# Kernel optimization log

Hardware: AMD Instinct MI355X
Metric: run time of the kernel (lower is better)

The kernel has to match this reference:

```python
import jax, jax.numpy as jnp
import numpy as np

N_NODES = 50000
N_EDGES = 800000
NFEAT = 96
NHID = 96
NCLASS = 40


def setup_inputs() -> dict:
    key = jax.random.key(0)
    ks = jax.random.split(key, 8)
    x = jax.random.normal(ks[0], (N_NODES, NFEAT), dtype=jnp.float32)
    edge_index = jax.random.randint(ks[1], (2, N_EDGES), 0, N_NODES, dtype=jnp.int64)
    def glorot(k, shape):
        fan_in = shape[1]
        bound = 1.0 / np.sqrt(fan_in)
        return jax.random.uniform(k, shape, jnp.float32, -bound, bound)
    return {
        'x': x,
        'edge_index': edge_index,
        'W1_l': glorot(ks[2], (NHID, NFEAT)),
        'b1_l': jnp.zeros((NHID,), jnp.float32),
        'W1_r': glorot(ks[3], (NHID, NFEAT)),
        'W2_l': glorot(ks[4], (NCLASS, NHID)),
        'b2_l': jnp.zeros((NCLASS,), jnp.float32),
        'W2_r': glorot(ks[5], (NCLASS, NHID)),
    }


def _sage_conv(x, src, dst, W_l, b_l, W_r):
    # gather neighbor features per edge, scatter-mean onto dst nodes
    msg = x[src]                                   # [E, F]
    agg = jax.ops.segment_sum(msg, dst, num_segments=N_NODES)   # [N, F]
    cnt = jax.ops.segment_sum(jnp.ones((src.shape[0],), x.dtype), dst,
                              num_segments=N_NODES)             # [N]
    agg = agg / jnp.maximum(cnt, 1.0)[:, None]
    # lin_l(agg) + lin_r(x)
    return agg @ W_l.T + b_l + x @ W_r.T


def reference(x, edge_index, W1_l, b1_l, W1_r, W2_l, b2_l, W2_r):
    src, dst = edge_index[0], edge_index[1]
    h = _sage_conv(x, src, dst, W1_l, b1_l, W1_r)
    h = jax.nn.relu(h)  # dropout is identity in eval mode
    h = _sage_conv(h, src, dst, W2_l, b2_l, W2_r)
    return jax.nn.log_softmax(h, axis=1)
```

## Files before the change

kernel.cpp:

```cpp
#include <hip/hip_runtime.h>
#include <hip/hip_fp8.h>
#include <math.h>

#define NCLASS 40
#define BSH    6
#define BSIZE  64
#define MAXB   1024
#define BCAP   2048
#define EPB    4096
#define LCOL   2048

typedef __attribute__((ext_vector_type(8))) short short8;
typedef __attribute__((ext_vector_type(4))) float float4v;
typedef __attribute__((ext_vector_type(2))) float float2v;

__device__ __forceinline__ unsigned short f2bf(float f) {
    union { float f; unsigned u; } v; v.f = f;
    unsigned r = v.u + 0x7fffu + ((v.u >> 16) & 1u);
    return (unsigned short)(r >> 16);
}
__device__ __forceinline__ float bf2f(unsigned int s) {
    union { unsigned u; float f; } v; v.u = s << 16; return v.f;
}
__device__ __forceinline__ void acc_fp8x4(unsigned int v, float* a) {
#if __has_builtin(__builtin_amdgcn_cvt_pk_f32_fp8)
    float2v lo = __builtin_amdgcn_cvt_pk_f32_fp8((int)v, false);
    float2v hi = __builtin_amdgcn_cvt_pk_f32_fp8((int)v, true);
    a[0] += lo[0]; a[1] += lo[1]; a[2] += hi[0]; a[3] += hi[1];
#else
    #pragma unroll
    for (int k = 0; k < 4; ++k) {
        __hip_fp8_e4m3 q8; q8.__x = (__hip_fp8_storage_t)((v >> (8 * k)) & 0xffu);
        a[k] += (float)q8;
    }
#endif
}

__global__ __launch_bounds__(256) void convhist_kernel(const int* __restrict__ ei,
                                                       const float4* __restrict__ x4,
                                                       const float* __restrict__ W1l,
                                                       const float* __restrict__ W1r,
                                                       const float* __restrict__ W2l,
                                                       const float* __restrict__ W2r,
                                                       int* __restrict__ histT,
                                                       unsigned short* __restrict__ axb,
                                                       unsigned char* __restrict__ xq,
                                                       unsigned short* __restrict__ wb1,
                                                       unsigned short* __restrict__ wb2,
                                                       int N, int E, int nbucket,
                                                       int nbin, int xblocks) {
    __shared__ int hcnt[MAXB];
    int tid = threadIdx.x;
    int blk = blockIdx.x;
    if (blk < nbin) {
        for (int t = tid; t < nbucket; t += 256) hcnt[t] = 0;
        __syncthreads();
        int e0 = blk * EPB;
        for (int it = 0; it < EPB / 256; ++it) {
            int e = e0 + it * 256 + tid;
            if (e < E) atomicAdd(&hcnt[ei[E + e] >> BSH], 1);
        }
        __syncthreads();
        for (int t = tid; t < nbucket; t += 256)
            histT[t * nbin + blk] = hcnt[t];
        return;
    }
    if (blk < nbin + xblocks) {
        int idx = (blk - nbin) * 256 + tid;
        if (idx >= N * 24) return;
        int n = idx / 24, q = idx - n * 24;
        float4 v = x4[idx];
        ushort4 o;
        o.x = f2bf(v.x); o.y = f2bf(v.y); o.z = f2bf(v.z); o.w = f2bf(v.w);
        *(ushort4*)(axb + (size_t)n * 192 + 96 + q * 4) = o;
        __hip_fp8_e4m3 q0(v.x), q1(v.y), q2(v.z), q3(v.w);
        unsigned int pk = (unsigned)q0.__x | ((unsigned)q1.__x << 8)
                        | ((unsigned)q2.__x << 16) | ((unsigned)q3.__x << 24);
        *(unsigned int*)(xq + (size_t)n * 128 + q * 4) = pk;
        return;
    }
    int t = (blk - nbin - xblocks) * 256 + tid;
    const float* src;
    unsigned short* dst;
    if (t < 36 * 64) {
        int s = t >> 6, lane = t & 63;
        int kc = s / 6, jt = s - kc * 6;
        int j  = jt * 16 + (lane & 15);
        int k2 = kc * 32 + (lane >> 4) * 8;
        src = (k2 < 96) ? (W1l + j * 96 + k2) : (W1r + j * 96 + (k2 - 96));
        dst = wb1 + t * 8;
    } else if (t < 51 * 64) {
        int t2 = t - 36 * 64;
        int s = t2 >> 6, lane = t2 & 63;
        int kc = s / 5, jt = s - kc * 5;
        int j  = jt * 16 + (lane & 15);
        int k2 = kc * 32 + (lane >> 4) * 8;
        src = (j < 40) ? (W2l + j * 96 + k2) : (W2r + (j - 40) * 96 + k2);
        dst = wb2 + t2 * 8;
    } else return;
    ushort4 o0, o1;
    o0.x = f2bf(src[0]); o0.y = f2bf(src[1]); o0.z = f2bf(src[2]); o0.w = f2bf(src[3]);
    o1.x = f2bf(src[4]); o1.y = f2bf(src[5]); o1.z = f2bf(src[6]); o1.w = f2bf(src[7]);
    *(ushort4*)(dst)     = o0;
    *(ushort4*)(dst + 4) = o1;
}

__global__ __launch_bounds__(256) void bsum_kernel(int* __restrict__ histT,
                                                   int* __restrict__ gbh, int nbin) {
    __shared__ int s[256];
    int k = blockIdx.x, tid = threadIdx.x;
    int v = (tid < nbin) ? histT[k * nbin + tid] : 0;
    s[tid] = v;
    __syncthreads();
    for (int off = 1; off < 256; off <<= 1) {
        int o = (tid >= off) ? s[tid - off] : 0;
        __syncthreads();
        s[tid] += o;
        __syncthreads();
    }
    if (tid < nbin) histT[k * nbin + tid] = s[tid] - v;
    if (tid == 255) gbh[k] = s[255];
}

__global__ __launch_bounds__(256) void bin_kernel(const int* __restrict__ ei,
                                                  const int* __restrict__ histT,
                                                  unsigned int* __restrict__ tmp,
                                                  int E, int nbucket, int nbin) {
    __shared__ int lcnt[MAXB];
    __shared__ int lbase[MAXB];
    int tid = threadIdx.x;
    for (int t = tid; t < nbucket; t += 256) {
        lbase[t] = t * BCAP + histT[t * nbin + blockIdx.x];
        lcnt[t]  = 0;
    }
    __syncthreads();
    int e0 = blockIdx.x * EPB;
    for (int it = 0; it < EPB / 256; ++it) {
        int e = e0 + it * 256 + tid;
        if (e < E) {
            int src = ei[e], dst = ei[E + e];
            int b   = dst >> BSH;
            int ofs = atomicAdd(&lcnt[b], 1);
            tmp[lbase[b] + ofs] = (unsigned)src | ((unsigned)(dst & (BSIZE - 1)) << 16);
        }
    }
}

__global__ __launch_bounds__(256) void csr_agg_kernel(const unsigned int* __restrict__ tmp,
                                                      const int* __restrict__ gbh,
                                                      int* __restrict__ rp,
                                                      unsigned short* __restrict__ dg,
                                                      unsigned short* __restrict__ col,
                                                      const unsigned char* __restrict__ xq,
                                                      unsigned short* __restrict__ axb,
                                                      int N) {
    __shared__ int ncnt[BSIZE], nofs[BSIZE], sscan[BSIZE];
    __shared__ unsigned short lcol[LCOL];
    int b   = blockIdx.x;
    int tid = threadIdx.x;
    int s0  = b * BCAP;
    int cnt = gbh[b];
    int s1  = s0 + cnt;
    bool inl = (cnt <= LCOL);
    if (tid < BSIZE) ncnt[tid] = 0;
    __syncthreads();
    for (int i = s0 + tid; i < s1; i += 256)
        atomicAdd(&ncnt[tmp[i] >> 16], 1);
    __syncthreads();
    int v = (tid < BSIZE) ? ncnt[tid] : 0;
    if (tid < BSIZE) sscan[tid] = v;
    __syncthreads();
    for (int off = 1; off < BSIZE; off <<= 1) {
        int o = (tid < BSIZE && tid >= off) ? sscan[tid - off] : 0;
        __syncthreads();
        if (tid < BSIZE) sscan[tid] += o;
        __syncthreads();
    }
    if (tid < BSIZE) {
        nofs[tid] = sscan[tid] - v;
        int node = (b << BSH) + tid;
        if (node < N) { rp[node] = s0 + nofs[tid]; dg[node] = (unsigned short)v; }
        ncnt[tid] = 0;
    }
    __syncthreads();
    for (int i = s0 + tid; i < s1; i += 256) {
        unsigned int t2 = tmp[i];
        int d   = t2 >> 16;
        int ofs = atomicAdd(&ncnt[d], 1);
        int pos = nofs[d] + ofs;
        unsigned short sv = (unsigned short)(t2 & 0xffffu);
        col[s0 + pos] = sv;
        if (inl) lcol[pos] = sv;
    }
    __syncthreads();
    int nodebase = b << BSH;
    auto gather = [&](auto getc) {
        for (int item = tid; item < BSIZE * 6; item += 256) {
            int nl = item / 6;
            int q  = item - nl * 6;
            int ls  = nofs[nl];
            int deg = ncnt[nl];
            int le  = ls + deg;
            float a[16];
            #pragma unroll
            for (int k = 0; k < 16; ++k) a[k] = 0.f;
            int i = ls;
            for (; i + 3 < le; i += 4) {
                #pragma unroll
                for (int u = 0; u < 4; ++u) {
                    int c = getc(i + u);
                    uint4 w = *(const uint4*)(xq + (size_t)c * 128 + q * 16);
                    acc_fp8x4(w.x, a);
                    acc_fp8x4(w.y, a + 4);
                    acc_fp8x4(w.z, a + 8);
                    acc_fp8x4(w.w, a + 12);
                }
            }
            for (; i < le; ++i) {
                int c = getc(i);
                uint4 w = *(const uint4*)(xq + (size_t)c * 128 + q * 16);
                acc_fp8x4(w.x, a);
                acc_fp8x4(w.y, a + 4);
                acc_fp8x4(w.z, a + 8);
                acc_fp8x4(w.w, a + 12);
            }
            float inv = 1.0f / (float)(deg > 1 ? deg : 1);
            ushort4 o0, o1, o2, o3;
            o0.x = f2bf(a[0] * inv);  o0.y = f2bf(a[1] * inv);
            o0.z = f2bf(a[2] * inv);  o0.w = f2bf(a[3] * inv);
            o1.x = f2bf(a[4] * inv);  o1.y = f2bf(a[5] * inv);
            o1.z = f2bf(a[6] * inv);  o1.w = f2bf(a[7] * inv);
            o2.x = f2bf(a[8] * inv);  o2.y = f2bf(a[9] * inv);
            o2.z = f2bf(a[10] * inv); o2.w = f2bf(a[11] * inv);
            o3.x = f2bf(a[12] * inv); o3.y = f2bf(a[13] * inv);
            o3.z = f2bf(a[14] * inv); o3.w = f2bf(a[15] * inv);
            unsigned short* dst = axb + (size_t)(nodebase + nl) * 192 + q * 16;
            *(ushort4*)(dst)      = o0;
            *(ushort4*)(dst + 4)  = o1;
            *(ushort4*)(dst + 8)  = o2;
            *(ushort4*)(dst + 12) = o3;
        }
    };
    if (inl) gather([&](int i) { return (int)lcol[i]; });
    else     gather([&](int i) { return (int)col[s0 + i]; });
}

__global__ __launch_bounds__(256) void l1proj_kernel(const unsigned short* __restrict__ axb,
                                                     const unsigned short* __restrict__ wb1,
                                                     const float* __restrict__ b1,
                                                     const unsigned short* __restrict__ wb2,
                                                     const float* __restrict__ b2,
                                                     unsigned short* __restrict__ pl,
                                                     float* __restrict__ pr,
                                                     int N) {
    __shared__ unsigned short sh[128 * 104];
    int wave = threadIdx.x >> 6, lane = threadIdx.x & 63;
    int nbase = blockIdx.x * 128 + wave * 32;
    int lbase = wave * 32;
    int mrow = lane & 15, quad = lane >> 4;

    {
        float4v acc[2][6] = {};
        const short8* W = (const short8*)wb1;
        #pragma unroll
        for (int kc = 0; kc < 6; ++kc) {
            short8 a0 = *(const short8*)(axb + (size_t)(nbase + mrow)      * 192 + kc * 32 + quad * 8);
            short8 a1 = *(const short8*)(axb + (size_t)(nbase + 16 + mrow) * 192 + kc * 32 + quad * 8);
            #pragma unroll
            for (int jt = 0; jt < 6; ++jt) {
                short8 b = W[(kc * 6 + jt) * 64 + lane];
                acc[0][jt] = __builtin_amdgcn_mfma_f32_16x16x32_bf16(a0, b, acc[0][jt], 0, 0, 0);
                acc[1][jt] = __builtin_amdgcn_mfma_f32_16x16x32_bf16(a1, b, acc[1][jt], 0, 0, 0);
            }
        }
        #pragma unroll
        for (int jt = 0; jt < 6; ++jt) {
            int j = jt * 16 + mrow;
            float bj = b1[j];
            #pragma unroll
            for (int mt = 0; mt < 2; ++mt) {
                #pragma unroll
                for (int r = 0; r < 4; ++r) {
                    int nl = lbase + mt * 16 + quad * 4 + r;
                    sh[nl * 104 + j] = f2bf(fmaxf(acc[mt][jt][r] + bj, 0.f));
                }
            }
        }
    }
    __syncthreads();
    {
        float4v acc[2][5] = {};
        const short8* W = (const short8*)wb2;
        #pragma unroll
        for (int kc = 0; kc < 3; ++kc) {
            short8 a0 = *(const short8*)&sh[(lbase + mrow)      * 104 + kc * 32 + quad * 8];
            short8 a1 = *(const short8*)&sh[(lbase + 16 + mrow) * 104 + kc * 32 + quad * 8];
            #pragma unroll
            for (int jt = 0; jt < 5; ++jt) {
                short8 b = W[(kc * 5 + jt) * 64 + lane];
                acc[0][jt] = __builtin_amdgcn_mfma_f32_16x16x32_bf16(a0, b, acc[0][jt], 0, 0, 0);
                acc[1][jt] = __builtin_amdgcn_mfma_f32_16x16x32_bf16(a1, b, acc[1][jt], 0, 0, 0);
            }
        }
        #pragma unroll
        for (int jt = 0; jt < 5; ++jt) {
            int j = jt * 16 + mrow;
            float b2v = (j >= 40) ? b2[j - 40] : 0.f;
            #pragma unroll
            for (int mt = 0; mt < 2; ++mt) {
                #pragma unroll
                for (int r = 0; r < 4; ++r) {
                    int node = nbase + mt * 16 + quad * 4 + r;
                    if (node < N) {
                        float v = acc[mt][jt][r];
                        if (j < 40) pl[(size_t)node * 64 + j] = f2bf(v);
                        else        pr[(size_t)node * 40 + (j - 40)] = v + b2v;
                    }
                }
            }
        }
    }
}

__global__ __launch_bounds__(256) void final_kernel(const unsigned short* __restrict__ pl,
                                                    const float* __restrict__ pr,
                                                    const int* __restrict__ rp,
                                                    const unsigned short* __restrict__ dg,
                                                    const unsigned short* __restrict__ col,
                                                    float* __restrict__ out, int N) {
    __shared__ float red[4][6][40];
    int wave = threadIdx.x >> 6;
    int lane = threadIdx.x & 63;
    int n = blockIdx.x * 4 + wave;
    if (n >= N) return;
    int s = rp[n];
    int deg = dg[n];
    int e = s + deg;
    int g = lane / 10;
    int c = lane - g * 10;
    bool gok = (g < 6);
    float a0 = 0.f, a1 = 0.f, a2 = 0.f, a3 = 0.f;
    for (int base = s; base < e; base += 6) {
        int idx = base + g;
        if (gok && idx < e) {
            int cn = col[idx];
            uint2 u = *(const uint2*)(pl + (size_t)cn * 64 + c * 4);
            a0 += bf2f(u.x & 0xffffu); a1 += bf2f(u.x >> 16);
            a2 += bf2f(u.y & 0xffffu); a3 += bf2f(u.y >> 16);
        }
    }
    if (gok) {
        float4 t; t.x = a0; t.y = a1; t.z = a2; t.w = a3;
        *(float4*)&red[wave][g][c * 4] = t;
    }
    bool act = (lane < NCLASS);
    float v = -INFINITY;
    if (act) {
        float val = 0.f;
        #pragma unroll
        for (int gg = 0; gg < 6; ++gg) val += red[wave][gg][lane];
        float inv = 1.0f / (float)(deg > 1 ? deg : 1);
        v = val * inv + pr[(size_t)n * 40 + lane];
    }
    float m = v;
    #pragma unroll
    for (int off = 32; off >= 1; off >>= 1) m = fmaxf(m, __shfl_xor(m, off));
    float ex = act ? __expf(v - m) : 0.f;
    float ssum = ex;
    #pragma unroll
    for (int off = 32; off >= 1; off >>= 1) ssum += __shfl_xor(ssum, off);
    if (act) out[(size_t)n * 40 + lane] = v - m - __logf(ssum);
}

extern "C" void kernel_launch(void* const* d_in, const int* in_sizes, int n_in,
                              void* d_out, int out_size, void* d_ws, size_t ws_size,
                              hipStream_t stream) {
    const float* x   = (const float*)d_in[0];
    const int*   ei  = (const int*)  d_in[1];
    const float* W1l = (const float*)d_in[2];
    const float* b1  = (const float*)d_in[3];
    const float* W1r = (const float*)d_in[4];
    const float* W2l = (const float*)d_in[5];
    const float* b2  = (const float*)d_in[6];
    const float* W2r = (const float*)d_in[7];
    float* out = (float*)d_out;

    const int N = in_sizes[0] / 96;
    const int E = in_sizes[1] / 2;
    const int nbucket = (N + BSIZE - 1) >> BSH;
    const int nbin = (E + EPB - 1) / EPB;
    const int NB   = (N + 127) / 128;
    const int NP2  = NB * 128;
    const int xblocks = (N * 24 + 255) / 256;

    auto al = [](size_t v) { return (v + 255) & ~(size_t)255; };
    char* ws = (char*)d_ws;
    size_t o = 0;
    int* histT = (int*)(ws + o); o = al(o + (size_t)MAXB * 256 * 4);
    int* gbh   = (int*)(ws + o); o = al(o + (size_t)MAXB * 4);
    int* rp    = (int*)(ws + o); o = al(o + (size_t)N * 4);
    unsigned short* dg = (unsigned short*)(ws + o);  o = al(o + (size_t)N * 2);
    unsigned int*   tmp = (unsigned int*)(ws + o);   o = al(o + (size_t)MAXB * BCAP * 4);
    unsigned short* col = (unsigned short*)(ws + o); o = al(o + (size_t)MAXB * BCAP * 2);
    unsigned short* axb = (unsigned short*)(ws + o); o = al(o + (size_t)NP2 * 192 * 2);
    unsigned char*  xq  = (unsigned char*)(ws + o);  o = al(o + (size_t)NP2 * 128);
    unsigned short* wb1 = (unsigned short*)(ws + o); o = al(o + 36 * 64 * 8 * 2);
    unsigned short* wb2 = (unsigned short*)(ws + o); o = al(o + 15 * 64 * 8 * 2);
    unsigned short* pl  = (unsigned short*)(ws + o); o = al(o + (size_t)NP2 * 64 * 2);
    float*          pr  = (float*)(ws + o);          o = al(o + (size_t)N * 40 * 4);

    convhist_kernel<<<nbin + xblocks + 13, 256, 0, stream>>>(
        ei, (const float4*)x, W1l, W1r, W2l, W2r, histT, axb, xq, wb1, wb2,
        N, E, nbucket, nbin, xblocks);
    bsum_kernel<<<nbucket, 256, 0, stream>>>(histT, gbh, nbin);
    bin_kernel <<<nbin, 256, 0, stream>>>(ei, histT, tmp, E, nbucket, nbin);
    csr_agg_kernel<<<nbucket, 256, 0, stream>>>(tmp, gbh, rp, dg, col, xq, axb, N);
    l1proj_kernel<<<NB, 256, 0, stream>>>(axb, wb1, b1, wb2, b2, pl, pr, N);
    final_kernel<<<(N + 3) / 4, 256, 0, stream>>>(pl, pr, rp, dg, col, out, N);
}
```

Before: 166.9 us.

## Fuse layer-1 projection into CSR aggregation kernel via shared-memory staging

Merges the l1proj kernel into csr_agg, so the bf16 mean-aggregated features stay in shared memory and feed the MFMA projection directly. This drops the global round trip of the 192-wide axb buffer and one kernel launch; the x half is now stored as a separate 96-wide bf16 array. FP8 accumulation also switches to packed float2 adds. The trade-off is more shared memory per block and 64-row MFMA tiles instead of 128, which may lower occupancy and per-block weight reuse.

```diff
diff --git a/kernel.cpp b/kernel.cpp
--- a/kernel.cpp
+++ b/kernel.cpp
@@ -22,18 +22,9 @@
 __device__ __forceinline__ float bf2f(unsigned int s) {
     union { unsigned u; float f; } v; v.u = s << 16; return v.f;
 }
-__device__ __forceinline__ void acc_fp8x4(unsigned int v, float* a) {
-#if __has_builtin(__builtin_amdgcn_cvt_pk_f32_fp8)
-    float2v lo = __builtin_amdgcn_cvt_pk_f32_fp8((int)v, false);
-    float2v hi = __builtin_amdgcn_cvt_pk_f32_fp8((int)v, true);
-    a[0] += lo[0]; a[1] += lo[1]; a[2] += hi[0]; a[3] += hi[1];
-#else
-    #pragma unroll
-    for (int k = 0; k < 4; ++k) {
-        __hip_fp8_e4m3 q8; q8.__x = (__hip_fp8_storage_t)((v >> (8 * k)) & 0xffu);
-        a[k] += (float)q8;
-    }
-#endif
+__device__ __forceinline__ void acc_fp8x4p(unsigned int v, float2v* a2) {
+    a2[0] += __builtin_amdgcn_cvt_pk_f32_fp8((int)v, false);
+    a2[1] += __builtin_amdgcn_cvt_pk_f32_fp8((int)v, true);
 }
 
 __global__ __launch_bounds__(256) void convhist_kernel(const int* __restrict__ ei,
@@ -43,7 +34,7 @@
                                                        const float* __restrict__ W2l,
                                                        const float* __restrict__ W2r,
                                                        int* __restrict__ histT,
-                                                       unsigned short* __restrict__ axb,
+                                                       unsigned short* __restrict__ xb,
                                                        unsigned char* __restrict__ xq,
                                                        unsigned short* __restrict__ wb1,
                                                        unsigned short* __restrict__ wb2,
@@ -72,7 +63,7 @@
         float4 v = x4[idx];
         ushort4 o;
         o.x = f2bf(v.x); o.y = f2bf(v.y); o.z = f2bf(v.z); o.w = f2bf(v.w);
-        *(ushort4*)(axb + (size_t)n * 192 + 96 + q * 4) = o;
+        *(ushort4*)(xb + (size_t)n * 96 + q * 4) = o;
         __hip_fp8_e4m3 q0(v.x), q1(v.y), q2(v.z), q3(v.w);
         unsigned int pk = (unsigned)q0.__x | ((unsigned)q1.__x << 8)
                         | ((unsigned)q2.__x << 16) | ((unsigned)q3.__x << 24);
@@ -146,16 +137,24 @@
     }
 }
 
-__global__ __launch_bounds__(256) void csr_agg_kernel(const unsigned int* __restrict__ tmp,
-                                                      const int* __restrict__ gbh,
-                                                      int* __restrict__ rp,
-                                                      unsigned short* __restrict__ dg,
-                                                      unsigned short* __restrict__ col,
-                                                      const unsigned char* __restrict__ xq,
-                                                      unsigned short* __restrict__ axb,
-                                                      int N) {
+__global__ __launch_bounds__(256) void csr_agg_mm_kernel(const unsigned int* __restrict__ tmp,
+                                                         const int* __restrict__ gbh,
+                                                         int* __restrict__ rp,
+                                                         unsigned short* __restrict__ dg,
+                                                         unsigned short* __restrict__ col,
+                                                         const unsigned char* __restrict__ xq,
+                                                         const unsigned short* __restrict__ xb,
+                                                         const unsigned short* __restrict__ wb1,
+                                                         const float* __restrict__ b1,
+                                                         const unsigned short* __restrict__ wb2,
+                                                         const float* __restrict__ b2,
+                                                         unsigned short* __restrict__ pl,
+                                                         float* __restrict__ pr,
+                                                         int N) {
     __shared__ int ncnt[BSIZE], nofs[BSIZE], sscan[BSIZE];
     __shared__ unsigned short lcol[LCOL];
+    __shared__ unsigned short sagg[BSIZE * 104];
+    __shared__ unsigned short sh[BSIZE * 104];
     int b   = blockIdx.x;
     int tid = threadIdx.x;
     int s0  = b * BCAP;
@@ -193,7 +192,6 @@
         if (inl) lcol[pos] = sv;
     }
     __syncthreads();
-    int nodebase = b << BSH;
     auto gather = [&](auto getc) {
         for (int item = tid; item < BSIZE * 6; item += 256) {
             int nl = item / 6;
@@ -201,40 +199,40 @@
             int ls  = nofs[nl];
             int deg = ncnt[nl];
             int le  = ls + deg;
-            float a[16];
-            #pragma unroll
-            for (int k = 0; k < 16; ++k) a[k] = 0.f;
+            float2v a2[8];
+            #pragma unroll
+            for (int k = 0; k < 8; ++k) a2[k] = float2v{0.f, 0.f};
             int i = ls;
             for (; i + 3 < le; i += 4) {
                 #pragma unroll
                 for (int u = 0; u < 4; ++u) {
                     int c = getc(i + u);
                     uint4 w = *(const uint4*)(xq + (size_t)c * 128 + q * 16);
-                    acc_fp8x4(w.x, a);
-                    acc_fp8x4(w.y, a + 4);
-                    acc_fp8x4(w.z, a + 8);
-                    acc_fp8x4(w.w, a + 12);
+                    acc_fp8x4p(w.x, a2);
+                    acc_fp8x4p(w.y, a2 + 2);
+                    acc_fp8x4p(w.z, a2 + 4);
+                    acc_fp8x4p(w.w, a2 + 6);
                 }
             }
             for (; i < le; ++i) {
                 int c = getc(i);
                 uint4 w = *(const uint4*)(xq + (size_t)c * 128 + q * 16);
-                acc_fp8x4(w.x, a);
-                acc_fp8x4(w.y, a + 4);
-                acc_fp8x4(w.z, a + 8);
-                acc_fp8x4(w.w, a + 12);
+                acc_fp8x4p(w.x, a2);
+                acc_fp8x4p(w.y, a2 + 2);
+                acc_fp8x4p(w.z, a2 + 4);
+                acc_fp8x4p(w.w, a2 + 6);
             }
             float inv = 1.0f / (float)(deg > 1 ? deg : 1);
             ushort4 o0, o1, o2, o3;
-            o0.x = f2bf(a[0] * inv);  o0.y = f2bf(a[1] * inv);
-            o0.z = f2bf(a[2] * inv);  o0.w = f2bf(a[3] * inv);
-            o1.x = f2bf(a[4] * inv);  o1.y = f2bf(a[5] * inv);
-            o1.z = f2bf(a[6] * inv);  o1.w = f2bf(a[7] * inv);
-            o2.x = f2bf(a[8] * inv);  o2.y = f2bf(a[9] * inv);
-            o2.z = f2bf(a[10] * inv); o2.w = f2bf(a[11] * inv);
-            o3.x = f2bf(a[12] * inv); o3.y = f2bf(a[13] * inv);
-            o3.z = f2bf(a[14] * inv); o3.w = f2bf(a[15] * inv);
-            unsigned short* dst = axb + (size_t)(nodebase + nl) * 192 + q * 16;
+            o0.x = f2bf(a2[0][0] * inv); o0.y = f2bf(a2[0][1] * inv);
+            o0.z = f2bf(a2[1][0] * inv); o0.w = f2bf(a2[1][1] * inv);
+            o1.x = f2bf(a2[2][0] * inv); o1.y = f2bf(a2[2][1] * inv);
+            o1.z = f2bf(a2[3][0] * inv); o1.w = f2bf(a2[3][1] * inv);
+            o2.x = f2bf(a2[4][0] * inv); o2.y = f2bf(a2[4][1] * inv);
+            o2.z = f2bf(a2[5][0] * inv); o2.w = f2bf(a2[5][1] * inv);
+            o3.x = f2bf(a2[6][0] * inv); o3.y = f2bf(a2[6][1] * inv);
+            o3.z = f2bf(a2[7][0] * inv); o3.w = f2bf(a2[7][1] * inv);
+            unsigned short* dst = sagg + nl * 104 + q * 16;
             *(ushort4*)(dst)      = o0;
             *(ushort4*)(dst + 4)  = o1;
             *(ushort4*)(dst + 8)  = o2;
@@ -243,34 +241,24 @@
     };
     if (inl) gather([&](int i) { return (int)lcol[i]; });
     else     gather([&](int i) { return (int)col[s0 + i]; });
-}
-
-__global__ __launch_bounds__(256) void l1proj_kernel(const unsigned short* __restrict__ axb,
-                                                     const unsigned short* __restrict__ wb1,
-                                                     const float* __restrict__ b1,
-                                                     const unsigned short* __restrict__ wb2,
-                                                     const float* __restrict__ b2,
-                                                     unsigned short* __restrict__ pl,
-                                                     float* __restrict__ pr,
-                                                     int N) {
-    __shared__ unsigned short sh[128 * 104];
-    int wave = threadIdx.x >> 6, lane = threadIdx.x & 63;
-    int nbase = blockIdx.x * 128 + wave * 32;
-    int lbase = wave * 32;
+    __syncthreads();
+
+    int wave = tid >> 6, lane = tid & 63;
     int mrow = lane & 15, quad = lane >> 4;
-
+    int lrow = wave * 16 + mrow;
+    int nodebase = b << BSH;
     {
-        float4v acc[2][6] = {};
+        float4v acc[6] = {};
         const short8* W = (const short8*)wb1;
         #pragma unroll
         for (int kc = 0; kc < 6; ++kc) {
-            short8 a0 = *(const short8*)(axb + (size_t)(nbase + mrow)      * 192 + kc * 32 + quad * 8);
-            short8 a1 = *(const short8*)(axb + (size_t)(nbase + 16 + mrow) * 192 + kc * 32 + quad * 8);
+            short8 a0 = (kc < 3)
+                ? *(const short8*)&sagg[lrow * 104 + kc * 32 + quad * 8]
+                : *(const short8*)(xb + (size_t)(nodebase + lrow) * 96 + (kc - 3) * 32 + quad * 8);
             #pragma unroll
             for (int jt = 0; jt < 6; ++jt) {
-                short8 b = W[(kc * 6 + jt) * 64 + lane];
-                acc[0][jt] = __builtin_amdgcn_mfma_f32_16x16x32_bf16(a0, b, acc[0][jt], 0, 0, 0);
-                acc[1][jt] = __builtin_amdgcn_mfma_f32_16x16x32_bf16(a1, b, acc[1][jt], 0, 0, 0);
+                short8 bb = W[(kc * 6 + jt) * 64 + lane];
+                acc[jt] = __builtin_amdgcn_mfma_f32_16x16x32_bf16(a0, bb, acc[jt], 0, 0, 0);
             }
         }
         #pragma unroll
@@ -278,28 +266,23 @@
             int j = jt * 16 + mrow;
             float bj = b1[j];
             #pragma unroll
-            for (int mt = 0; mt < 2; ++mt) {
-                #pragma unroll
-                for (int r = 0; r < 4; ++r) {
-                    int nl = lbase + mt * 16 + quad * 4 + r;
-                    sh[nl * 104 + j] = f2bf(fmaxf(acc[mt][jt][r] + bj, 0.f));
-                }
+            for (int r = 0; r < 4; ++r) {
+                int nl = wave * 16 + quad * 4 + r;
+                sh[nl * 104 + j] = f2bf(fmaxf(acc[jt][r] + bj, 0.f));
             }
         }
     }
     __syncthreads();
     {
-        float4v acc[2][5] = {};
+        float4v acc[5] = {};
         const short8* W = (const short8*)wb2;
         #pragma unroll
         for (int kc = 0; kc < 3; ++kc) {
-            short8 a0 = *(const short8*)&sh[(lbase + mrow)      * 104 + kc * 32 + quad * 8];
-            short8 a1 = *(const short8*)&sh[(lbase + 16 + mrow) * 104 + kc * 32 + quad * 8];
+            short8 a0 = *(const short8*)&sh[lrow * 104 + kc * 32 + quad * 8];
             #pragma unroll
             for (int jt = 0; jt < 5; ++jt) {
-                short8 b = W[(kc * 5 + jt) * 64 + lane];
-                acc[0][jt] = __builtin_amdgcn_mfma_f32_16x16x32_bf16(a0, b, acc[0][jt], 0, 0, 0);
-                acc[1][jt] = __builtin_amdgcn_mfma_f32_16x16x32_bf16(a1, b, acc[1][jt], 0, 0, 0);
+                short8 bb = W[(kc * 5 + jt) * 64 + lane];
+                acc[jt] = __builtin_amdgcn_mfma_f32_16x16x32_bf16(a0, bb, acc[jt], 0, 0, 0);
             }
         }
         #pragma unroll
@@ -307,15 +290,12 @@
             int j = jt * 16 + mrow;
             float b2v = (j >= 40) ? b2[j - 40] : 0.f;
             #pragma unroll
-            for (int mt = 0; mt < 2; ++mt) {
-                #pragma unroll
-                for (int r = 0; r < 4; ++r) {
-                    int node = nbase + mt * 16 + quad * 4 + r;
-                    if (node < N) {
-                        float v = acc[mt][jt][r];
-                        if (j < 40) pl[(size_t)node * 64 + j] = f2bf(v);
-                        else        pr[(size_t)node * 40 + (j - 40)] = v + b2v;
-                    }
+            for (int r = 0; r < 4; ++r) {
+                int node = nodebase + wave * 16 + quad * 4 + r;
+                if (node < N) {
+                    float vv = acc[jt][r];
+                    if (j < 40) pl[(size_t)node * 64 + j] = f2bf(vv);
+                    else        pr[(size_t)node * 40 + (j - 40)] = vv + b2v;
                 }
             }
         }
@@ -389,8 +369,7 @@
     const int E = in_sizes[1] / 2;
     const int nbucket = (N + BSIZE - 1) >> BSH;
     const int nbin = (E + EPB - 1) / EPB;
-    const int NB   = (N + 127) / 128;
-    const int NP2  = NB * 128;
+    const int NP2  = nbucket * BSIZE;
     const int xblocks = (N * 24 + 255) / 256;
 
     auto al = [](size_t v) { return (v + 255) & ~(size_t)255; };
@@ -402,7 +381,7 @@
     unsigned short* dg = (unsigned short*)(ws + o);  o = al(o + (size_t)N * 2);
     unsigned int*   tmp = (unsigned int*)(ws + o);   o = al(o + (size_t)MAXB * BCAP * 4);
     unsigned short* col = (unsigned short*)(ws + o); o = al(o + (size_t)MAXB * BCAP * 2);
-    unsigned short* axb = (unsigned short*)(ws + o); o = al(o + (size_t)NP2 * 192 * 2);
+    unsigned short* xb  = (unsigned short*)(ws + o); o = al(o + (size_t)NP2 * 96 * 2);
     unsigned char*  xq  = (unsigned char*)(ws + o);  o = al(o + (size_t)NP2 * 128);
     unsigned short* wb1 = (unsigned short*)(ws + o); o = al(o + 36 * 64 * 8 * 2);
     unsigned short* wb2 = (unsigned short*)(ws + o); o = al(o + 15 * 64 * 8 * 2);
@@ -410,11 +389,11 @@
     float*          pr  = (float*)(ws + o);          o = al(o + (size_t)N * 40 * 4);
 
     convhist_kernel<<<nbin + xblocks + 13, 256, 0, stream>>>(
-        ei, (const float4*)x, W1l, W1r, W2l, W2r, histT, axb, xq, wb1, wb2,
+        ei, (const float4*)x, W1l, W1r, W2l, W2r, histT, xb, xq, wb1, wb2,
         N, E, nbucket, nbin, xblocks);
     bsum_kernel<<<nbucket, 256, 0, stream>>>(histT, gbh, nbin);
     bin_kernel <<<nbin, 256, 0, stream>>>(ei, histT, tmp, E, nbucket, nbin);
-    csr_agg_kernel<<<nbucket, 256, 0, stream>>>(tmp, gbh, rp, dg, col, xq, axb, N);
-    l1proj_kernel<<<NB, 256, 0, stream>>>(axb, wb1, b1, wb2, b2, pl, pr, N);
+    csr_agg_mm_kernel<<<nbucket, 256, 0, stream>>>(
+        tmp, gbh, rp, dg, col, xq, xb, wb1, b1, wb2, b2, pl, pr, N);
     final_kernel<<<(N + 3) / 4, 256, 0, stream>>>(pl, pr, rp, dg, col, out, N);
 }
```

Result: faster. 160.5 us (-3.8%).
